# Kernel optimization log

Measured on AMD Instinct MI355X. Metric: run time of the kernel, lower is better.

The kernel has to match this reference:

```python
import jax, jax.numpy as jnp
import numpy as np
import math

D = 1024
H = 16
NEG = -10000.0


def _layernorm(x, g, b, eps=1e-6):
    mu = x.mean(-1, keepdims=True)
    var = ((x - mu) ** 2).mean(-1, keepdims=True)
    return (x - mu) / jnp.sqrt(var + eps) * g + b


def _gelu(x):
    return x * 0.5 * (1.0 + jax.lax.erf(x / math.sqrt(2.0)))


def _split_heads(x):
    N, L, _ = x.shape
    return x.reshape(N, L, H, D // H).transpose(0, 2, 1, 3)  # (N,H,L,d)


def _attention(q, k, v, mask):
    # q,k,v: (N,Lq/Lk,D); mask: (N,1,Lq,Lk) of 0/1 or None
    d = D // H
    qh, kh, vh = _split_heads(q), _split_heads(k), _split_heads(v)
    scores = jnp.einsum('bhqd,bhkd->bhqk', qh, kh) / math.sqrt(d)
    if mask is not None:
        scores = scores + (1.0 - mask) * NEG
    probs = jax.nn.softmax(scores, axis=-1)
    ctx = jnp.einsum('bhqk,bhkd->bhqd', probs, vh)
    N, _, Lq, _ = ctx.shape
    ctx = ctx.transpose(0, 2, 1, 3).reshape(N, Lq, D)
    return ctx, scores.mean(1)  # attention_vis = masked scaled scores averaged over heads


def setup_inputs() -> dict:
    key = jax.random.key(0)
    ks = jax.random.split(key, 16)
    N, Lt, Lv = 16, 512, 512
    w = lambda k: (jax.random.normal(k, (D, D), jnp.float32) * 0.02)
    inp = {
        'dec_hidden_states': jax.random.normal(ks[0], (N, Lt, D), jnp.float32),
        'dec_mask': jnp.ones((N, Lt), jnp.float32),
        'enc_outputs': jax.random.normal(ks[1], (N, Lv, D), jnp.float32),
        'sa_wq': w(ks[2]), 'sa_bq': jnp.zeros((D,), jnp.float32),
        'sa_wk': w(ks[3]), 'sa_bk': jnp.zeros((D,), jnp.float32),
        'sa_wv': w(ks[4]), 'sa_bv': jnp.zeros((D,), jnp.float32),
        'n1_g': jnp.ones((D,), jnp.float32), 'n1_b': jnp.zeros((D,), jnp.float32),
        'ca_wq': w(ks[5]), 'ca_bq': jnp.zeros((D,), jnp.float32),
        'ca_wk': w(ks[6]), 'ca_bk': jnp.zeros((D,), jnp.float32),
        'ca_wv': w(ks[7]), 'ca_bv': jnp.zeros((D,), jnp.float32),
        'n2_g': jnp.ones((D,), jnp.float32), 'n2_b': jnp.zeros((D,), jnp.float32),
        'int_w': w(ks[8]), 'int_b': jnp.zeros((D,), jnp.float32),
        'out_w': w(ks[9]), 'out_b': jnp.zeros((D,), jnp.float32),
        'out_g': jnp.ones((D,), jnp.float32), 'out_beta': jnp.zeros((D,), jnp.float32),
    }
    return inp


def reference(dec_hidden_states, dec_mask, enc_outputs,
              sa_wq, sa_bq, sa_wk, sa_bk, sa_wv, sa_bv, n1_g, n1_b,
              ca_wq, ca_bq, ca_wk, ca_bk, ca_wv, ca_bv, n2_g, n2_b,
              int_w, int_b, out_w, out_b, out_g, out_beta):
    x = dec_hidden_states
    N, Lt, _ = x.shape
    # causal + padding mask: (N,1,Lt) * tril(Lt,Lt) -> (N,Lt,Lt) -> (N,1,Lt,Lt)
    causal = jnp.tril(jnp.ones((Lt, Lt), x.dtype))
    self_mask = (dec_mask[:, None, :] * causal)[:, None, :, :]
    # self attention
    q = x @ sa_wq + sa_bq
    k = x @ sa_wk + sa_bk
    v = x @ sa_wv + sa_bv
    sa_ctx, _ = _attention(q, k, v, self_mask)
    h = _layernorm(sa_ctx + x, n1_g, n1_b)
    # cross attention (no mask)
    cq = h @ ca_wq + ca_bq
    ck = enc_outputs @ ca_wk + ca_bk
    cv = enc_outputs @ ca_wv + ca_bv
    ca_ctx, attention_vis = _attention(cq, ck, cv, None)
    h2 = _layernorm(h + ca_ctx, n2_g, n2_b)
    # intermediate (gelu FFN)
    inter = _gelu(h2 @ int_w + int_b)
    # Output: dense + residual(intermediate itself, as in original) + LayerNorm
    out = _layernorm(inter @ out_w + out_b + inter, out_g, out_beta)
    return out, attention_vis
```

## Files before the change

kernel.cpp:

```cpp
#include <hip/hip_runtime.h>
#include <hip/hip_bf16.h>
#include <math.h>

#define DDIM 1024
#define NH   16
#define LTOK 512
#define NBATCH 16

typedef unsigned short u16;
typedef unsigned short u16x8 __attribute__((ext_vector_type(8)));
typedef unsigned short u16x4 __attribute__((ext_vector_type(4)));
typedef __bf16 bf16x8 __attribute__((ext_vector_type(8)));
typedef float f32x4 __attribute__((ext_vector_type(4)));

typedef __attribute__((address_space(1))) void as1_void;
typedef __attribute__((address_space(3))) void as3_void;

__device__ __forceinline__ void llds16(const u16* g, u16* l) {
    __builtin_amdgcn_global_load_lds((as1_void*)g, (as3_void*)l, 16, 0, 0);
}

__device__ __forceinline__ float bf2f(u16 u) {
    unsigned v = ((unsigned)u) << 16;
    float f; __builtin_memcpy(&f, &v, 4); return f;
}
__device__ __forceinline__ u16 f2bf(float f) {
    unsigned u; __builtin_memcpy(&u, &f, 4);
    u += 0x7fffu + ((u >> 16) & 1u);
    return (u16)(u >> 16);
}

struct GemmOp {
    const u16* A; const u16* B; u16* C; float* Cf; const float* bias;
    u16* VTp;
    long sA1, sA2, sB1, sB2, sC1, sC2;
    int lda, ldb, ldc, M, N, K, zdiv, flags, nblk, vtcol0;
    float scale;
};

template<int MODE>
__global__ __launch_bounds__(256) void gemm_bt_kernel(GemmOp o1, GemmOp o2)
{
    constexpr int NB   = (MODE == 0) ? 1 : 2;
    constexpr int BUFE = 128 * 32;
    __shared__ __align__(16) u16 As[NB * BUFE];
    __shared__ __align__(16) u16 Bs[NB * BUFE];

    const bool second = (int)blockIdx.x >= o1.nblk;
    const GemmOp& o = second ? o2 : o1;
    int bidx = blockIdx.x - (second ? o1.nblk : 0);

    const int tilesN = o.N >> 7;
    const int tilesM = o.M >> 7;
    const int tiles  = tilesM * tilesN;
    const int z = bidx / tiles;
    const int t = bidx - z * tiles;
    const int zb = z / o.zdiv, zh = z - zb * o.zdiv;

    int tm, tn;
    if ((tilesM & 7) == 0) {
        const int xcd = t & 7, idx = t >> 3;
        const int mg  = tilesM >> 3;
        tm = ((idx % mg) << 3) | xcd;
        tn = idx / mg;
    } else {
        tm = t / tilesN;
        tn = t - tm * tilesN;
    }
    const int m0 = tm << 7, n0 = tn << 7;

    const u16* Ab = o.A + (long)zb * o.sA1 + (long)zh * o.sA2;
    const u16* Bb = o.B + (long)zb * o.sB1 + (long)zh * o.sB2;
    u16*   Cb  = o.C  ? o.C  + (long)zb * o.sC1 + (long)zh * o.sC2 : nullptr;
    float* Cfb = o.Cf ? o.Cf + (long)zb * o.sC1 + (long)zh * o.sC2 : nullptr;

    const int tid  = threadIdx.x;
    const int lane = tid & 63;
    const int wave = tid >> 6;
    const int wm = (wave & 1) << 6, wn = (wave >> 1) << 6;
    const int quad = lane >> 4, l16 = lane & 15;

    f32x4 acc[4][4];
#pragma unroll
    for (int i = 0; i < 4; i++)
#pragma unroll
        for (int j = 0; j < 4; j++) acc[i][j] = (f32x4){0.f, 0.f, 0.f, 0.f};

    const int lrA = (wave << 5) + (lane >> 2);
    const int lc  = (lane & 3) << 3;
    const u16* gA0 = Ab + (long)(m0 + lrA) * o.lda + lc;
    const u16* gA1 = Ab + (long)(m0 + lrA + 16) * o.lda + lc;
    const u16* gB0 = Bb + (long)(n0 + lrA) * o.ldb + lc;
    const u16* gB1 = Bb + (long)(n0 + lrA + 16) * o.ldb + lc;
    u16* lA0 = As + ((wave << 5) +  0) * 32;
    u16* lA1 = As + ((wave << 5) + 16) * 32;
    u16* lB0 = Bs + ((wave << 5) +  0) * 32;
    u16* lB1 = Bs + ((wave << 5) + 16) * 32;

    auto STAGE = [&](int bi, int k0) {
        llds16(gA0 + k0, lA0 + bi * BUFE);
        llds16(gA1 + k0, lA1 + bi * BUFE);
        llds16(gB0 + k0, lB0 + bi * BUFE);
        llds16(gB1 + k0, lB1 + bi * BUFE);
    };
    auto COMPUTE = [&](int bi) {
        const u16* Ac = As + bi * BUFE;
        const u16* Bc = Bs + bi * BUFE;
        bf16x8 af[4], bfr[4];
#pragma unroll
        for (int t2 = 0; t2 < 4; t2++)
            af[t2] = *(const bf16x8*)(Ac + (wm + t2 * 16 + l16) * 32 + quad * 8);
#pragma unroll
        for (int t2 = 0; t2 < 4; t2++)
            bfr[t2] = *(const bf16x8*)(Bc + (wn + t2 * 16 + l16) * 32 + quad * 8);
#pragma unroll
        for (int i = 0; i < 4; i++)
#pragma unroll
            for (int j = 0; j < 4; j++)
                acc[i][j] = __builtin_amdgcn_mfma_f32_16x16x32_bf16(
                    bfr[j], af[i], acc[i][j], 0, 0, 0);
    };

    const int K = o.K;
    if (MODE == 0) {
        for (int k0 = 0; k0 < K; k0 += 32) {
            __syncthreads();
            STAGE(0, k0);
            __syncthreads();
            COMPUTE(0);
        }
    } else {
        STAGE(0, 0);
        __syncthreads();
        int cur = 0;
        for (int k0 = 0; k0 < K; k0 += 32) {
            const int nxt = cur ^ 1;
            if (k0 + 32 < K) STAGE(nxt, k0 + 32);
            COMPUTE(cur);
            __syncthreads();
            cur = nxt;
        }
    }

#pragma unroll
    for (int i = 0; i < 4; i++) {
        const long row = m0 + wm + i * 16 + l16;
#pragma unroll
        for (int j = 0; j < 4; j++) {
            const int col = n0 + wn + j * 16 + quad * 4;
            f32x4 bv = o.bias ? *(const f32x4*)(o.bias + col)
                              : (f32x4){0.f, 0.f, 0.f, 0.f};
            f32x4 v4;
#pragma unroll
            for (int r = 0; r < 4; r++) {
                float v = acc[i][j][r] * o.scale + bv[r];
                if (o.flags & 1)
                    v = 0.5f * v * (1.f + erff(v * 0.70710678118654752f));
                v4[r] = v;
            }
            if (o.VTp && col >= o.vtcol0) {
                const int dv  = col - o.vtcol0;
                const long bh = (row >> 9) * NH + (dv >> 6);
                const int tok = (int)(row & (LTOK - 1));
                u16* vp = o.VTp + (bh * 64 + (dv & 63)) * LTOK + tok;
#pragma unroll
                for (int r = 0; r < 4; r++)
                    vp[(long)r * LTOK] = f2bf(v4[r]);
            } else if (Cfb) {
                *(f32x4*)(Cfb + row * o.ldc + col) = v4;
            } else {
                u16x4 ov;
#pragma unroll
                for (int r = 0; r < 4; r++) ov[r] = f2bf(v4[r]);
                *(u16x4*)(Cb + row * o.ldc + col) = ov;
            }
        }
    }
}

__global__ __launch_bounds__(256, 4) void flash_kernel(
    const u16* __restrict__ Q, const u16* __restrict__ K,
    const u16* __restrict__ VT, u16* __restrict__ O,
    const float* __restrict__ mask, int causal, int ldq, int ldk)
{
    __shared__ __align__(16) u16 Ks[128 * 72];
    __shared__ __align__(16) u16 Vs[64 * 136];
    const int tid  = threadIdx.x;
    const int wave = tid >> 6, lane = tid & 63;
    const int quad = lane >> 4, l16 = lane & 15;
    const int bh = blockIdx.x, qt = blockIdx.y, b = bh >> 4, h = bh & 15;
    const int qbase = qt * 64 + wave * 16;
    const int qrow  = qbase + l16;

    const u16* qp = Q + ((long)b * LTOK + qrow) * ldq + h * 64 + quad * 8;
    bf16x8 aq0 = *(const bf16x8*)(qp);
    bf16x8 aq1 = *(const bf16x8*)(qp + 32);

    f32x4 oacc[4];
#pragma unroll
    for (int jd = 0; jd < 4; jd++) oacc[jd] = (f32x4){0.f, 0.f, 0.f, 0.f};
    float m_st = -3.0e38f;
    float l_st = 0.f;

    const int krow = tid >> 3,       kcol = (tid & 7) << 3;
    const int vrow = tid >> 2,       vcol = (tid & 3) << 3;
    const u16* gK = K + ((long)b * LTOK + krow) * ldk + h * 64 + kcol;
    const u16* gV = VT + ((long)bh * 64 + vrow) * LTOK + vcol;

    const float C1    = 0.125f * 1.44269504088896340736f;
    const float NEGL2 = -10000.0f * 1.44269504088896340736f;

    const int nkt = causal ? ((qt * 64 + 63) >> 7) + 1 : (LTOK >> 7);

    u16x8 KR[4], VR[4];
#pragma unroll
    for (int i = 0; i < 4; i++) KR[i] = *(const u16x8*)(gK + (long)(i * 32) * ldk);
#pragma unroll
    for (int i = 0; i < 4; i++) VR[i] = *(const u16x8*)(gV + i * 32);
#pragma unroll
    for (int i = 0; i < 4; i++)
        *(u16x8*)(Ks + (i * 32 + krow) * 72 + kcol) = KR[i];
#pragma unroll
    for (int i = 0; i < 4; i++)
        *(u16x8*)(Vs + vrow * 136 + i * 32 + vcol) = VR[i];
    __syncthreads();

    for (int kt = 0; kt < nkt; kt++) {
        const int k0 = kt << 7;
        const bool more = (kt + 1 < nkt);

        if (more) {
            const int kn = k0 + 128;
#pragma unroll
            for (int i = 0; i < 4; i++)
                KR[i] = *(const u16x8*)(gK + (long)(kn + i * 32) * ldk);
#pragma unroll
            for (int i = 0; i < 4; i++)
                VR[i] = *(const u16x8*)(gV + kn + i * 32);
        }

        f32x4 s[8];
#pragma unroll
        for (int j = 0; j < 8; j++) {
            bf16x8 bk0 = *(const bf16x8*)(Ks + (j * 16 + l16) * 72 + quad * 8);
            bf16x8 bk1 = *(const bf16x8*)(Ks + (j * 16 + l16) * 72 + 32 + quad * 8);
            f32x4 z = (f32x4){0.f, 0.f, 0.f, 0.f};
            z = __builtin_amdgcn_mfma_f32_16x16x32_bf16(bk0, aq0, z, 0, 0, 0);
            s[j] = __builtin_amdgcn_mfma_f32_16x16x32_bf16(bk1, aq1, z, 0, 0, 0);
        }

        float tm0 = -3.0e38f, tm1 = -3.0e38f, tm2 = -3.0e38f, tm3 = -3.0e38f;
#pragma unroll
        for (int j = 0; j < 8; j++) {
            if (causal) {
                f32x4 m4 = *(const f32x4*)(mask + (long)b * LTOK + k0 + j * 16 + quad * 4);
#pragma unroll
                for (int r = 0; r < 4; r++) {
                    int key = k0 + j * 16 + quad * 4 + r;
                    float ad = (key <= qrow) ? fmaf(m4[r], -NEGL2, NEGL2) : NEGL2;
                    s[j][r] = fmaf(s[j][r], C1, ad);
                }
            } else {
#pragma unroll
                for (int r = 0; r < 4; r++) s[j][r] *= C1;
            }
            tm0 = fmaxf(tm0, s[j][0]); tm1 = fmaxf(tm1, s[j][1]);
            tm2 = fmaxf(tm2, s[j][2]); tm3 = fmaxf(tm3, s[j][3]);
        }
        float tmax = fmaxf(fmaxf(tm0, tm1), fmaxf(tm2, tm3));
        tmax = fmaxf(tmax, __shfl_xor(tmax, 16));
        tmax = fmaxf(tmax, __shfl_xor(tmax, 32));

        float mnew  = fmaxf(m_st, tmax);
        float alpha = __builtin_amdgcn_exp2f(m_st - mnew);
        m_st = mnew;

        float rs0 = 0.f, rs1 = 0.f, rs2 = 0.f, rs3 = 0.f;
        unsigned pk[8][2];
#pragma unroll
        for (int j = 0; j < 8; j++) {
            float p0 = __builtin_amdgcn_exp2f(s[j][0] - mnew);
            float p1 = __builtin_amdgcn_exp2f(s[j][1] - mnew);
            float p2 = __builtin_amdgcn_exp2f(s[j][2] - mnew);
            float p3 = __builtin_amdgcn_exp2f(s[j][3] - mnew);
            rs0 += p0; rs1 += p1; rs2 += p2; rs3 += p3;
            asm("v_cvt_pk_bf16_f32 %0, %1, %2" : "=v"(pk[j][0]) : "v"(p0), "v"(p1));
            asm("v_cvt_pk_bf16_f32 %0, %1, %2" : "=v"(pk[j][1]) : "v"(p2), "v"(p3));
        }
        float rsum = (rs0 + rs1) + (rs2 + rs3);
        rsum += __shfl_xor(rsum, 16);
        rsum += __shfl_xor(rsum, 32);
        l_st = l_st * alpha + rsum;

#pragma unroll
        for (int jd = 0; jd < 4; jd++) oacc[jd] *= alpha;

#pragma unroll
        for (int kk = 0; kk < 4; kk++) {
            unsigned wv[4] = { pk[2 * kk][0], pk[2 * kk][1],
                               pk[2 * kk + 1][0], pk[2 * kk + 1][1] };
            bf16x8 bp; __builtin_memcpy(&bp, wv, 16);
#pragma unroll
            for (int jd = 0; jd < 4; jd++) {
                const u16* vb = Vs + (jd * 16 + l16) * 136 + kk * 32 + quad * 4;
                u16 va[8];
                *(u16x4*)(va)     = *(const u16x4*)(vb);
                *(u16x4*)(va + 4) = *(const u16x4*)(vb + 16);
                bf16x8 av; __builtin_memcpy(&av, va, 16);
                oacc[jd] = __builtin_amdgcn_mfma_f32_16x16x32_bf16(av, bp, oacc[jd], 0, 0, 0);
            }
        }

        if (more) {
            __syncthreads();
#pragma unroll
            for (int i = 0; i < 4; i++)
                *(u16x8*)(Ks + (i * 32 + krow) * 72 + kcol) = KR[i];
#pragma unroll
            for (int i = 0; i < 4; i++)
                *(u16x8*)(Vs + vrow * 136 + i * 32 + vcol) = VR[i];
            __syncthreads();
        }
    }

    float linv = 1.f / l_st;
    long obase = ((long)b * LTOK + qrow) * DDIM + h * 64;
#pragma unroll
    for (int jd = 0; jd < 4; jd++) {
        u16x4 ov;
#pragma unroll
        for (int r = 0; r < 4; r++) ov[r] = f2bf(oacc[jd][r] * linv);
        *(u16x4*)(O + obase + jd * 16 + quad * 4) = ov;
    }
}

__global__ __launch_bounds__(256) void add_ln_kernel(
    const u16* __restrict__ a, const u16* __restrict__ b,
    const float* __restrict__ b32,
    const float* __restrict__ g, const float* __restrict__ bt,
    u16* __restrict__ o, float* __restrict__ of)
{
    long row = blockIdx.x;
    int tid = threadIdx.x;
    __shared__ float red[4];
    const u16* ar = a + row * DDIM;
    float xv[4]; float s = 0.f;
#pragma unroll
    for (int i = 0; i < 4; i++) {
        int c = tid + 256 * i;
        float sum = bf2f(ar[c]) + (b32 ? b32[row * DDIM + c] : bf2f(b[row * DDIM + c]));
        xv[i] = fminf(fmaxf(sum, -1.0e18f), 1.0e18f);
        s += xv[i];
    }
#pragma unroll
    for (int ofs = 32; ofs >= 1; ofs >>= 1) s += __shfl_xor(s, ofs);
    int wave = tid >> 6, lane = tid & 63;
    if (lane == 0) red[wave] = s;
    __syncthreads();
    float mu = (red[0] + red[1] + red[2] + red[3]) * (1.f / 1024.f);
    __syncthreads();
    float v = 0.f;
#pragma unroll
    for (int i = 0; i < 4; i++) { float d = xv[i] - mu; v += d * d; }
#pragma unroll
    for (int ofs = 32; ofs >= 1; ofs >>= 1) v += __shfl_xor(v, ofs);
    if (lane == 0) red[wave] = v;
    __syncthreads();
    float var = (red[0] + red[1] + red[2] + red[3]) * (1.f / 1024.f);
    float inv = rsqrtf(var + 1e-6f);
#pragma unroll
    for (int i = 0; i < 4; i++) {
        int c = tid + 256 * i;
        float r = (xv[i] - mu) * inv * g[c] + bt[c];
        if (of) of[row * DDIM + c] = r;
        else    o [row * DDIM + c] = f2bf(r);
    }
}

__global__ __launch_bounds__(256) void cvt2_kernel(
    const float* __restrict__ s0, u16* __restrict__ d0,
    const float* __restrict__ s1, u16* __restrict__ d1)
{
    const float* src = blockIdx.y ? s1 : s0;
    u16* dst = blockIdx.y ? d1 : d0;
    long i = ((long)blockIdx.x * 256 + threadIdx.x) * 8;
    u16x8 o;
#pragma unroll
    for (int j = 0; j < 8; j++) o[j] = f2bf(src[i + j]);
    *(u16x8*)(dst + i) = o;
}

__global__ __launch_bounds__(256) void wt_kernel(
    const float* w0, const float* w1, const float* w2, const float* w3,
    const float* w4, const float* w5, const float* w6, const float* w7,
    u16* __restrict__ wt)
{
    const float* srcs[8] = {w0, w1, w2, w3, w4, w5, w6, w7};
    const float* w = srcs[blockIdx.z];
    u16* o = wt + (long)blockIdx.z * DDIM * DDIM;
    __shared__ u16 t[32][33];
    int tx = threadIdx.x & 31, ty = threadIdx.x >> 5;
    int c0 = blockIdx.x << 5, r0 = blockIdx.y << 5;
#pragma unroll
    for (int i = 0; i < 4; i++)
        t[ty + 8 * i][tx] = f2bf(w[(long)(r0 + ty + 8 * i) * DDIM + c0 + tx]);
    __syncthreads();
#pragma unroll
    for (int i = 0; i < 4; i++)
        o[(long)(c0 + ty + 8 * i) * DDIM + r0 + tx] = t[tx][ty + 8 * i];
}

__global__ __launch_bounds__(256) void biascat_kernel(
    const float* __restrict__ b0, const float* __restrict__ b1,
    const float* __restrict__ b2, float* __restrict__ dst)
{
    int i = blockIdx.x * 256 + threadIdx.x;
    const float* s = (i < 1024) ? b0 : (i < 2048) ? b1 : b2;
    dst[i] = s[i & 1023];
}

extern "C" void kernel_launch(void* const* d_in, const int* in_sizes, int n_in,
                              void* d_out, int out_size, void* d_ws, size_t ws_size,
                              hipStream_t stream)
{
    const float* x     = (const float*)d_in[0];
    const float* dmsk  = (const float*)d_in[1];
    const float* enc   = (const float*)d_in[2];
    const float* sa_wq = (const float*)d_in[3];  const float* sa_bq = (const float*)d_in[4];
    const float* sa_wk = (const float*)d_in[5];  const float* sa_bk = (const float*)d_in[6];
    const float* sa_wv = (const float*)d_in[7];  const float* sa_bv = (const float*)d_in[8];
    const float* n1_g  = (const float*)d_in[9];  const float* n1_b  = (const float*)d_in[10];
    const float* ca_wq = (const float*)d_in[11]; const float* ca_bq = (const float*)d_in[12];
    const float* ca_wk = (const float*)d_in[13]; const float* ca_bk = (const float*)d_in[14];
    const float* ca_wv = (const float*)d_in[15]; const float* ca_bv = (const float*)d_in[16];
    const float* n2_g  = (const float*)d_in[17]; const float* n2_b  = (const float*)d_in[18];
    const float* int_w = (const float*)d_in[19]; const float* int_b = (const float*)d_in[20];
    const float* out_w = (const float*)d_in[21]; const float* out_b = (const float*)d_in[22];
    const float* out_g = (const float*)d_in[23]; const float* out_bt= (const float*)d_in[24];

    float* outp = (float*)d_out;
    float* visp = outp + (long)NBATCH * LTOK * DDIM;

    const size_t WTB  = (size_t)8 * DDIM * DDIM * 2;
    const size_t BUF1 = (size_t)LTOK * DDIM * 2;
    int cb = 16;
    while (cb > 1 && WTB + (size_t)cb * 7 * BUF1 + 32768 > ws_size)
        cb >>= 1;

    char* ws = (char*)d_ws;
    size_t off = 0;
    auto alloc = [&](size_t bytes) -> u16* {
        u16* p = (u16*)(ws + off);
        off += (bytes + 255) & ~(size_t)255;
        return p;
    };
    u16* Xb  = alloc((size_t)cb * BUF1);
    u16* Eb  = alloc((size_t)cb * BUF1);
    u16* Q3  = alloc((size_t)cb * 3 * BUF1);
    u16* Vt  = alloc((size_t)cb * BUF1);
    u16* Cx  = alloc((size_t)cb * BUF1);
    u16* WT  = alloc(WTB);
    float* biasQKV = (float*)alloc(3072 * sizeof(float));
    float* biasKV  = (float*)alloc(2048 * sizeof(float));

    u16* Wsaq = WT + 0L * DDIM * DDIM;
    u16* Wcaq = WT + 3L * DDIM * DDIM;
    u16* Wcak = WT + 4L * DDIM * DDIM;
    u16* Wint = WT + 6L * DDIM * DDIM;
    u16* Wout = WT + 7L * DDIM * DDIM;

    auto mkop = [](const u16* A, int lda, const u16* B, int ldb,
                   u16* C, float* Cf, int ldc, int M, int N, int K,
                   const float* bias, float scale, int flags) -> GemmOp {
        GemmOp o{};
        o.A = A; o.B = B; o.C = C; o.Cf = Cf; o.bias = bias;
        o.VTp = nullptr; o.vtcol0 = 0;
        o.sA1 = 0; o.sA2 = 0; o.sB1 = 0; o.sB2 = 0; o.sC1 = 0; o.sC2 = 0;
        o.lda = lda; o.ldb = ldb; o.ldc = ldc; o.M = M; o.N = N; o.K = K;
        o.zdiv = 1; o.flags = flags; o.nblk = (M / 128) * (N / 128);
        o.scale = scale;
        return o;
    };

    auto launch = [&](int mode, GemmOp o1, GemmOp o2) {
        int nb = o1.nblk + o2.nblk;
        if (mode == 0)
            gemm_bt_kernel<0><<<dim3(nb), dim3(256), 0, stream>>>(o1, o2);
        else
            gemm_bt_kernel<1><<<dim3(nb), dim3(256), 0, stream>>>(o1, o2);
    };
    GemmOp nil{};

    const long SLD = (long)LTOK * DDIM;
    const long SSC = (long)LTOK * LTOK;

    wt_kernel<<<dim3(32, 32, 8), dim3(256), 0, stream>>>(
        sa_wq, sa_wk, sa_wv, ca_wq, ca_wk, ca_wv, int_w, out_w, WT);
    biascat_kernel<<<dim3(12), dim3(256), 0, stream>>>(sa_bq, sa_bk, sa_bv, biasQKV);
    biascat_kernel<<<dim3(8),  dim3(256), 0, stream>>>(ca_bk, ca_bv, ca_bv, biasKV);

    for (int b0 = 0; b0 < NBATCH; b0 += cb) {
        const float* xc = x   + (long)b0 * SLD;
        const float* ec = enc + (long)b0 * SLD;
        const int M = cb * LTOK;
        const int Z = cb * NH;
        const int cvtg = (int)(((long)M * DDIM) / (256 * 8));

        u16* h   = Xb;
        u16* CQ  = Q3;
        u16* CKV = Q3 + (size_t)cb * LTOK * DDIM;
        u16* I   = Vt;
        u16* G   = Cx;
        u16* h2  = Eb;

        cvt2_kernel<<<dim3(cvtg, 2), dim3(256), 0, stream>>>(xc, Xb, ec, Eb);

        {
            GemmOp o = mkop(Xb, DDIM, Wsaq, DDIM, Q3, nullptr, 3 * DDIM,
                            M, 3 * DDIM, DDIM, biasQKV, 1.f, 0);
            o.VTp = Vt; o.vtcol0 = 2 * DDIM;
            launch(0, o, nil);
        }

        flash_kernel<<<dim3(Z, 8), dim3(256), 0, stream>>>(
            Q3, Q3 + DDIM, Vt, Cx, dmsk + (long)b0 * LTOK, 1, 3 * DDIM, 3 * DDIM);

        add_ln_kernel<<<dim3(M), dim3(256), 0, stream>>>(
            Cx, nullptr, xc, n1_g, n1_b, h, nullptr);

        {
            GemmOp okv = mkop(Eb, DDIM, Wcak, DDIM, CKV, nullptr, 2 * DDIM,
                              M, 2 * DDIM, DDIM, biasKV, 1.f, 0);
            okv.VTp = Vt; okv.vtcol0 = DDIM;
            launch(1, mkop(h, DDIM, Wcaq, DDIM, CQ, nullptr, DDIM,
                           M, DDIM, DDIM, ca_bq, 1.f, 0), okv);
        }

        flash_kernel<<<dim3(Z, 8), dim3(256), 0, stream>>>(
            CQ, CKV, Vt, Cx, nullptr, 0, DDIM, 2 * DDIM);

        add_ln_kernel<<<dim3(M), dim3(256), 0, stream>>>(
            h, Cx, nullptr, n2_g, n2_b, h2, nullptr);

        GemmOp ovis{};
        ovis.A = CQ;  ovis.lda = DDIM;     ovis.sA1 = SLD;               ovis.sA2 = 0;
        ovis.B = CKV; ovis.ldb = 2 * DDIM; ovis.sB1 = (long)LTOK * 2 * DDIM; ovis.sB2 = 0;
        ovis.C = nullptr; ovis.Cf = visp + (long)b0 * SSC;
        ovis.VTp = nullptr; ovis.vtcol0 = 0;
        ovis.ldc = LTOK; ovis.sC1 = SSC; ovis.sC2 = 0;
        ovis.M = LTOK; ovis.N = LTOK; ovis.K = DDIM; ovis.zdiv = 1;
        ovis.bias = nullptr; ovis.scale = 1.f / 128.f; ovis.flags = 0;
        ovis.nblk = (LTOK / 128) * (LTOK / 128) * cb;
        launch(1, ovis,
               mkop(h2, DDIM, Wint, DDIM, I, nullptr, DDIM,
                    M, DDIM, DDIM, int_b, 1.f, 1));

        launch(1, mkop(I, DDIM, Wout, DDIM, G, nullptr, DDIM,
                       M, DDIM, DDIM, out_b, 1.f, 0), nil);

        add_ln_kernel<<<dim3(M), dim3(256), 0, stream>>>(
            G, I, nullptr, out_g, out_bt, nullptr, outp + (long)b0 * SLD);
    }
}
```

Baseline: 548.8 us.

## Process two 16-row query tiles per wave in flash attention

Each wave in the flash attention kernel now handles 32 query rows instead of 16, so every K/V tile staged in LDS feeds twice as many MFMAs. The grid shrinks to 4 query blocks of 128 rows, and the causal tile count becomes qt+1. The aim is less LDS and global K/V traffic per unit of work, at the cost of more registers (launch bounds lowered to 2), fewer blocks, and more wasted work on the causal diagonal tiles. The QKV projection GEMM also switches from template mode 0 to mode 1.

Result: faster. 533.4 us (-2.8%).

```diff
diff --git a/kernel.cpp b/kernel.cpp
--- a/kernel.cpp
+++ b/kernel.cpp
@@ -178,7 +178,7 @@
     }
 }
 
-__global__ __launch_bounds__(256, 4) void flash_kernel(
+__global__ __launch_bounds__(256, 2) void flash_kernel(
     const u16* __restrict__ Q, const u16* __restrict__ K,
     const u16* __restrict__ VT, u16* __restrict__ O,
     const float* __restrict__ mask, int causal, int ldq, int ldk)
@@ -189,18 +189,25 @@
     const int wave = tid >> 6, lane = tid & 63;
     const int quad = lane >> 4, l16 = lane & 15;
     const int bh = blockIdx.x, qt = blockIdx.y, b = bh >> 4, h = bh & 15;
-    const int qbase = qt * 64 + wave * 16;
-    const int qrow  = qbase + l16;
-
-    const u16* qp = Q + ((long)b * LTOK + qrow) * ldq + h * 64 + quad * 8;
-    bf16x8 aq0 = *(const bf16x8*)(qp);
-    bf16x8 aq1 = *(const bf16x8*)(qp + 32);
-
-    f32x4 oacc[4];
-#pragma unroll
-    for (int jd = 0; jd < 4; jd++) oacc[jd] = (f32x4){0.f, 0.f, 0.f, 0.f};
-    float m_st = -3.0e38f;
-    float l_st = 0.f;
+    const int qbase = qt * 128 + wave * 32;
+    const int qrow0 = qbase + l16;
+    const int qrow1 = qbase + 16 + l16;
+
+    const u16* qp0 = Q + ((long)b * LTOK + qrow0) * ldq + h * 64 + quad * 8;
+    const u16* qp1 = qp0 + (long)16 * ldq;
+    bf16x8 aq00 = *(const bf16x8*)(qp0);
+    bf16x8 aq01 = *(const bf16x8*)(qp0 + 32);
+    bf16x8 aq10 = *(const bf16x8*)(qp1);
+    bf16x8 aq11 = *(const bf16x8*)(qp1 + 32);
+
+    f32x4 oacc0[4], oacc1[4];
+#pragma unroll
+    for (int jd = 0; jd < 4; jd++) {
+        oacc0[jd] = (f32x4){0.f, 0.f, 0.f, 0.f};
+        oacc1[jd] = (f32x4){0.f, 0.f, 0.f, 0.f};
+    }
+    float m0_ = -3.0e38f, m1_ = -3.0e38f;
+    float l0_ = 0.f, l1_ = 0.f;
 
     const int krow = tid >> 3,       kcol = (tid & 7) << 3;
     const int vrow = tid >> 2,       vcol = (tid & 3) << 3;
@@ -210,7 +217,7 @@
     const float C1    = 0.125f * 1.44269504088896340736f;
     const float NEGL2 = -10000.0f * 1.44269504088896340736f;
 
-    const int nkt = causal ? ((qt * 64 + 63) >> 7) + 1 : (LTOK >> 7);
+    const int nkt = causal ? (qt + 1) : (LTOK >> 7);
 
     u16x8 KR[4], VR[4];
 #pragma unroll
@@ -239,17 +246,21 @@
                 VR[i] = *(const u16x8*)(gV + kn + i * 32);
         }
 
-        f32x4 s[8];
+        f32x4 s0[8], s1[8];
 #pragma unroll
         for (int j = 0; j < 8; j++) {
             bf16x8 bk0 = *(const bf16x8*)(Ks + (j * 16 + l16) * 72 + quad * 8);
             bf16x8 bk1 = *(const bf16x8*)(Ks + (j * 16 + l16) * 72 + 32 + quad * 8);
-            f32x4 z = (f32x4){0.f, 0.f, 0.f, 0.f};
-            z = __builtin_amdgcn_mfma_f32_16x16x32_bf16(bk0, aq0, z, 0, 0, 0);
-            s[j] = __builtin_amdgcn_mfma_f32_16x16x32_bf16(bk1, aq1, z, 0, 0, 0);
-        }
-
-        float tm0 = -3.0e38f, tm1 = -3.0e38f, tm2 = -3.0e38f, tm3 = -3.0e38f;
+            f32x4 z0 = (f32x4){0.f, 0.f, 0.f, 0.f};
+            z0 = __builtin_amdgcn_mfma_f32_16x16x32_bf16(bk0, aq00, z0, 0, 0, 0);
+            s0[j] = __builtin_amdgcn_mfma_f32_16x16x32_bf16(bk1, aq01, z0, 0, 0, 0);
+            f32x4 z1 = (f32x4){0.f, 0.f, 0.f, 0.f};
+            z1 = __builtin_amdgcn_mfma_f32_16x16x32_bf16(bk0, aq10, z1, 0, 0, 0);
+            s1[j] = __builtin_amdgcn_mfma_f32_16x16x32_bf16(bk1, aq11, z1, 0, 0, 0);
+        }
+
+        float ta0 = -3.0e38f, ta1 = -3.0e38f, ta2 = -3.0e38f, ta3 = -3.0e38f;
+        float tb0 = -3.0e38f, tb1 = -3.0e38f, tb2 = -3.0e38f, tb3 = -3.0e38f;
 #pragma unroll
         for (int j = 0; j < 8; j++) {
             if (causal) {
@@ -257,49 +268,75 @@
 #pragma unroll
                 for (int r = 0; r < 4; r++) {
                     int key = k0 + j * 16 + quad * 4 + r;
-                    float ad = (key <= qrow) ? fmaf(m4[r], -NEGL2, NEGL2) : NEGL2;
-                    s[j][r] = fmaf(s[j][r], C1, ad);
+                    float adm = fmaf(m4[r], -NEGL2, NEGL2);
+                    s0[j][r] = fmaf(s0[j][r], C1, (key <= qrow0) ? adm : NEGL2);
+                    s1[j][r] = fmaf(s1[j][r], C1, (key <= qrow1) ? adm : NEGL2);
                 }
             } else {
 #pragma unroll
-                for (int r = 0; r < 4; r++) s[j][r] *= C1;
+                for (int r = 0; r < 4; r++) { s0[j][r] *= C1; s1[j][r] *= C1; }
             }
-            tm0 = fmaxf(tm0, s[j][0]); tm1 = fmaxf(tm1, s[j][1]);
-            tm2 = fmaxf(tm2, s[j][2]); tm3 = fmaxf(tm3, s[j][3]);
-        }
-        float tmax = fmaxf(fmaxf(tm0, tm1), fmaxf(tm2, tm3));
-        tmax = fmaxf(tmax, __shfl_xor(tmax, 16));
-        tmax = fmaxf(tmax, __shfl_xor(tmax, 32));
-
-        float mnew  = fmaxf(m_st, tmax);
-        float alpha = __builtin_amdgcn_exp2f(m_st - mnew);
-        m_st = mnew;
-
-        float rs0 = 0.f, rs1 = 0.f, rs2 = 0.f, rs3 = 0.f;
-        unsigned pk[8][2];
+            ta0 = fmaxf(ta0, s0[j][0]); ta1 = fmaxf(ta1, s0[j][1]);
+            ta2 = fmaxf(ta2, s0[j][2]); ta3 = fmaxf(ta3, s0[j][3]);
+            tb0 = fmaxf(tb0, s1[j][0]); tb1 = fmaxf(tb1, s1[j][1]);
+            tb2 = fmaxf(tb2, s1[j][2]); tb3 = fmaxf(tb3, s1[j][3]);
+        }
+        float tmax0 = fmaxf(fmaxf(ta0, ta1), fmaxf(ta2, ta3));
+        float tmax1 = fmaxf(fmaxf(tb0, tb1), fmaxf(tb2, tb3));
+        tmax0 = fmaxf(tmax0, __shfl_xor(tmax0, 16));
+        tmax0 = fmaxf(tmax0, __shfl_xor(tmax0, 32));
+        tmax1 = fmaxf(tmax1, __shfl_xor(tmax1, 16));
+        tmax1 = fmaxf(tmax1, __shfl_xor(tmax1, 32));
+
+        float mn0 = fmaxf(m0_, tmax0);
+        float mn1 = fmaxf(m1_, tmax1);
+        float al0 = __builtin_amdgcn_exp2f(m0_ - mn0);
+        float al1 = __builtin_amdgcn_exp2f(m1_ - mn1);
+        m0_ = mn0; m1_ = mn1;
+
+        unsigned pk0[8][2], pk1[8][2];
+        float ra0 = 0.f, ra1 = 0.f, ra2 = 0.f, ra3 = 0.f;
 #pragma unroll
         for (int j = 0; j < 8; j++) {
-            float p0 = __builtin_amdgcn_exp2f(s[j][0] - mnew);
-            float p1 = __builtin_amdgcn_exp2f(s[j][1] - mnew);
-            float p2 = __builtin_amdgcn_exp2f(s[j][2] - mnew);
-            float p3 = __builtin_amdgcn_exp2f(s[j][3] - mnew);
-            rs0 += p0; rs1 += p1; rs2 += p2; rs3 += p3;
-            asm("v_cvt_pk_bf16_f32 %0, %1, %2" : "=v"(pk[j][0]) : "v"(p0), "v"(p1));
-            asm("v_cvt_pk_bf16_f32 %0, %1, %2" : "=v"(pk[j][1]) : "v"(p2), "v"(p3));
-        }
-        float rsum = (rs0 + rs1) + (rs2 + rs3);
-        rsum += __shfl_xor(rsum, 16);
-        rsum += __shfl_xor(rsum, 32);
-        l_st = l_st * alpha + rsum;
-
-#pragma unroll
-        for (int jd = 0; jd < 4; jd++) oacc[jd] *= alpha;
+            float p0 = __builtin_amdgcn_exp2f(s0[j][0] - mn0);
+            float p1 = __builtin_amdgcn_exp2f(s0[j][1] - mn0);
+            float p2 = __builtin_amdgcn_exp2f(s0[j][2] - mn0);
+            float p3 = __builtin_amdgcn_exp2f(s0[j][3] - mn0);
+            ra0 += p0; ra1 += p1; ra2 += p2; ra3 += p3;
+            asm("v_cvt_pk_bf16_f32 %0, %1, %2" : "=v"(pk0[j][0]) : "v"(p0), "v"(p1));
+            asm("v_cvt_pk_bf16_f32 %0, %1, %2" : "=v"(pk0[j][1]) : "v"(p2), "v"(p3));
+        }
+        float rsum0 = (ra0 + ra1) + (ra2 + ra3);
+        float rb0 = 0.f, rb1 = 0.f, rb2 = 0.f, rb3 = 0.f;
+#pragma unroll
+        for (int j = 0; j < 8; j++) {
+            float p0 = __builtin_amdgcn_exp2f(s1[j][0] - mn1);
+            float p1 = __builtin_amdgcn_exp2f(s1[j][1] - mn1);
+            float p2 = __builtin_amdgcn_exp2f(s1[j][2] - mn1);
+            float p3 = __builtin_amdgcn_exp2f(s1[j][3] - mn1);
+            rb0 += p0; rb1 += p1; rb2 += p2; rb3 += p3;
+            asm("v_cvt_pk_bf16_f32 %0, %1, %2" : "=v"(pk1[j][0]) : "v"(p0), "v"(p1));
+            asm("v_cvt_pk_bf16_f32 %0, %1, %2" : "=v"(pk1[j][1]) : "v"(p2), "v"(p3));
+        }
+        float rsum1 = (rb0 + rb1) + (rb2 + rb3);
+        rsum0 += __shfl_xor(rsum0, 16);
+        rsum0 += __shfl_xor(rsum0, 32);
+        rsum1 += __shfl_xor(rsum1, 16);
+        rsum1 += __shfl_xor(rsum1, 32);
+        l0_ = l0_ * al0 + rsum0;
+        l1_ = l1_ * al1 + rsum1;
+
+#pragma unroll
+        for (int jd = 0; jd < 4; jd++) { oacc0[jd] *= al0; oacc1[jd] *= al1; }
 
 #pragma unroll
         for (int kk = 0; kk < 4; kk++) {
-            unsigned wv[4] = { pk[2 * kk][0], pk[2 * kk][1],
-                               pk[2 * kk + 1][0], pk[2 * kk + 1][1] };
-            bf16x8 bp; __builtin_memcpy(&bp, wv, 16);
+            unsigned wv0[4] = { pk0[2 * kk][0], pk0[2 * kk][1],
+                                pk0[2 * kk + 1][0], pk0[2 * kk + 1][1] };
+            unsigned wv1[4] = { pk1[2 * kk][0], pk1[2 * kk][1],
+                                pk1[2 * kk + 1][0], pk1[2 * kk + 1][1] };
+            bf16x8 bp0; __builtin_memcpy(&bp0, wv0, 16);
+            bf16x8 bp1; __builtin_memcpy(&bp1, wv1, 16);
 #pragma unroll
             for (int jd = 0; jd < 4; jd++) {
                 const u16* vb = Vs + (jd * 16 + l16) * 136 + kk * 32 + quad * 4;
@@ -307,7 +344,8 @@
                 *(u16x4*)(va)     = *(const u16x4*)(vb);
                 *(u16x4*)(va + 4) = *(const u16x4*)(vb + 16);
                 bf16x8 av; __builtin_memcpy(&av, va, 16);
-                oacc[jd] = __builtin_amdgcn_mfma_f32_16x16x32_bf16(av, bp, oacc[jd], 0, 0, 0);
+                oacc0[jd] = __builtin_amdgcn_mfma_f32_16x16x32_bf16(av, bp0, oacc0[jd], 0, 0, 0);
+                oacc1[jd] = __builtin_amdgcn_mfma_f32_16x16x32_bf16(av, bp1, oacc1[jd], 0, 0, 0);
             }
         }
 
@@ -323,14 +361,20 @@
         }
     }
 
-    float linv = 1.f / l_st;
-    long obase = ((long)b * LTOK + qrow) * DDIM + h * 64;
+    float li0 = 1.f / l0_;
+    float li1 = 1.f / l1_;
+    long obase0 = ((long)b * LTOK + qrow0) * DDIM + h * 64;
+    long obase1 = obase0 + (long)16 * DDIM;
 #pragma unroll
     for (int jd = 0; jd < 4; jd++) {
-        u16x4 ov;
-#pragma unroll
-        for (int r = 0; r < 4; r++) ov[r] = f2bf(oacc[jd][r] * linv);
-        *(u16x4*)(O + obase + jd * 16 + quad * 4) = ov;
+        u16x4 ov0, ov1;
+#pragma unroll
+        for (int r = 0; r < 4; r++) {
+            ov0[r] = f2bf(oacc0[jd][r] * li0);
+            ov1[r] = f2bf(oacc1[jd][r] * li1);
+        }
+        *(u16x4*)(O + obase0 + jd * 16 + quad * 4) = ov0;
+        *(u16x4*)(O + obase1 + jd * 16 + quad * 4) = ov1;
     }
 }
 
@@ -482,12 +526,9 @@
         return o;
     };
 
-    auto launch = [&](int mode, GemmOp o1, GemmOp o2) {
+    auto launch = [&](GemmOp o1, GemmOp o2) {
         int nb = o1.nblk + o2.nblk;
-        if (mode == 0)
-            gemm_bt_kernel<0><<<dim3(nb), dim3(256), 0, stream>>>(o1, o2);
-        else
-            gemm_bt_kernel<1><<<dim3(nb), dim3(256), 0, stream>>>(o1, o2);
+        gemm_bt_kernel<1><<<dim3(nb), dim3(256), 0, stream>>>(o1, o2);
     };
     GemmOp nil{};
 
@@ -519,10 +560,10 @@
             GemmOp o = mkop(Xb, DDIM, Wsaq, DDIM, Q3, nullptr, 3 * DDIM,
                             M, 3 * DDIM, DDIM, biasQKV, 1.f, 0);
             o.VTp = Vt; o.vtcol0 = 2 * DDIM;
-            launch(0, o, nil);
-        }
-
-        flash_kernel<<<dim3(Z, 8), dim3(256), 0, stream>>>(
+            launch(o, nil);
+        }
+
+        flash_kernel<<<dim3(Z, 4), dim3(256), 0, stream>>>(
             Q3, Q3 + DDIM, Vt, Cx, dmsk + (long)b0 * LTOK, 1, 3 * DDIM, 3 * DDIM);
 
         add_ln_kernel<<<dim3(M), dim3(256), 0, stream>>>(
@@ -532,11 +573,11 @@
             GemmOp okv = mkop(Eb, DDIM, Wcak, DDIM, CKV, nullptr, 2 * DDIM,
                               M, 2 * DDIM, DDIM, biasKV, 1.f, 0);
             okv.VTp = Vt; okv.vtcol0 = DDIM;
-            launch(1, mkop(h, DDIM, Wcaq, DDIM, CQ, nullptr, DDIM,
-                           M, DDIM, DDIM, ca_bq, 1.f, 0), okv);
-        }
-
-        flash_kernel<<<dim3(Z, 8), dim3(256), 0, stream>>>(
+            launch(mkop(h, DDIM, Wcaq, DDIM, CQ, nullptr, DDIM,
+                        M, DDIM, DDIM, ca_bq, 1.f, 0), okv);
+        }
+
+        flash_kernel<<<dim3(Z, 4), dim3(256), 0, stream>>>(
             CQ, CKV, Vt, Cx, nullptr, 0, DDIM, 2 * DDIM);
 
         add_ln_kernel<<<dim3(M), dim3(256), 0, stream>>>(
@@ -551,12 +592,12 @@
         ovis.M = LTOK; ovis.N = LTOK; ovis.K = DDIM; ovis.zdiv = 1;
         ovis.bias = nullptr; ovis.scale = 1.f / 128.f; ovis.flags = 0;
         ovis.nblk = (LTOK / 128) * (LTOK / 128) * cb;
-        launch(1, ovis,
+        launch(ovis,
                mkop(h2, DDIM, Wint, DDIM, I, nullptr, DDIM,
                     M, DDIM, DDIM, int_b, 1.f, 1));
 
-        launch(1, mkop(I, DDIM, Wout, DDIM, G, nullptr, DDIM,
-                       M, DDIM, DDIM, out_b, 1.f, 0), nil);
+        launch(mkop(I, DDIM, Wout, DDIM, G, nullptr, DDIM,
+                    M, DDIM, DDIM, out_b, 1.f, 0), nil);
 
         add_ln_kernel<<<dim3(M), dim3(256), 0, stream>>>(
             G, I, nullptr, out_g, out_bt, nullptr, outp + (long)b0 * SLD);
```
